# Optimization experiments

Measured on AMD Instinct MI355X. Metric: run time of the kernel, lower is better.

## Reference

```python
import jax, jax.numpy as jnp
import numpy as np

RANGE_MIN = -5.0
RANGE_MAX = 5.0
NBINS = 32
N, D = 1 << 20, 64
MIN_SLOPE = 1e-8


def setup_inputs() -> dict:
    key = jax.random.key(0)
    k1, k2, k3, k4 = jax.random.split(key, 4)
    interval = RANGE_MAX - RANGE_MIN
    min_bin_width = interval / NBINS / 100.0  # __init__ default
    # samples, mostly inside [range_min, range_max]
    x = (jax.random.normal(k1, (N, D), jnp.float32) * 2.0)
    # constrained params, produced exactly as the TransformedVariable bijectors do:
    # bin widths/heights: Shift(min_bin_width) o Scale(interval - mbw*nbins) o SoftmaxCentered
    def softmax_centered(u):
        pad = jnp.zeros(u.shape[:-1] + (1,), u.dtype)
        return jax.nn.softmax(jnp.concatenate([u, pad], axis=-1), axis=-1)
    scale = interval - min_bin_width * NBINS
    uw = 0.1 * jax.random.normal(k2, (D, NBINS - 1))
    uh = 0.1 * jax.random.normal(k3, (D, NBINS - 1))
    us = 0.01 * jax.random.normal(k4, (D, NBINS - 1))
    bin_widths = (min_bin_width + scale * softmax_centered(uw)).astype(jnp.float32)   # [D, nbins]
    bin_heights = (min_bin_width + scale * softmax_centered(uh)).astype(jnp.float32)  # [D, nbins]
    knot_slopes = (MIN_SLOPE + jax.nn.softplus(us)).astype(jnp.float32)               # [D, nbins-1]
    return {"x": x, "bin_widths": bin_widths, "bin_heights": bin_heights,
            "knot_slopes": knot_slopes}


def _spline_1d(x, kx, ky, kd):
    """Rational-quadratic spline forward for one dimension.
    x: [N]; kx, ky: [nbins+1] knot positions; kd: [nbins+1] knot slopes."""
    nbins = kx.shape[0] - 1
    # bin index k s.t. kx[k] <= x < kx[k+1]
    idx = jnp.clip(jnp.searchsorted(kx, x, side='right') - 1, 0, nbins - 1)
    xk, xk1 = kx[idx], kx[idx + 1]
    yk, yk1 = ky[idx], ky[idx + 1]
    dk, dk1 = kd[idx], kd[idx + 1]
    w = xk1 - xk
    h = yk1 - yk
    s = h / w                      # bin mean slope
    t = (x - xk) / w               # relative position in bin
    tt = t * (1.0 - t)
    num = h * (s * t * t + dk * tt)
    den = s + (dk1 + dk - 2.0 * s) * tt
    y = yk + num / den
    # TFP: identity outside [range_min, range_max]
    inside = (x >= kx[0]) & (x <= kx[-1])
    return jnp.where(inside, y, x)


def reference(x, bin_widths, bin_heights, knot_slopes):
    d = x.shape[-1]
    zeros = jnp.zeros((d, 1), x.dtype)
    ones = jnp.ones((d, 1), x.dtype)
    kx = RANGE_MIN + jnp.concatenate([zeros, jnp.cumsum(bin_widths, axis=-1)], axis=-1)   # [D, nbins+1]
    ky = RANGE_MIN + jnp.concatenate([zeros, jnp.cumsum(bin_heights, axis=-1)], axis=-1)  # [D, nbins+1]
    kd = jnp.concatenate([ones, knot_slopes, ones], axis=-1)  # boundary slopes fixed to 1
    return jax.vmap(_spline_1d, in_axes=(1, 0, 0, 0), out_axes=1)(x, kx, ky, kd)
```

## Files before the change

### kernel.cpp

```cpp
#include <hip/hip_runtime.h>

#define NBINS 32
#define DIM 64
#define RANGE_MIN_F (-5.0f)
#define RANGE_MAX_F (5.0f)
#define NCELL 64
#define LUT_STRIDE 68
#define BLOCK 512
#define GRID 768
#define INV_CW 6.4f
#define GBIAS 32.0f

typedef float f32x4 __attribute__((ext_vector_type(4)));


__global__ __launch_bounds__(BLOCK, 6) void rqs_fused(
        const float* __restrict__ x,
        const float* __restrict__ bw,
        const float* __restrict__ bh,
        const float* __restrict__ ks,
        float* __restrict__ out,
        int total) {
    __shared__ float4 s_recA[DIM * NBINS];
    __shared__ float2 s_kd2[DIM * NBINS];
    __shared__ unsigned char s_lut[DIM * LUT_STRIDE];

    const int t = threadIdx.x;

    if (t < DIM) {
        const int d = t;
        const int sw = d >> 2;
        float accw = 0.0f, acch = 0.0f;
        #pragma unroll
        for (int k = 0; k < NBINS; ++k) {
            float w = bw[d * NBINS + k];
            float h = bh[d * NBINS + k];
            s_recA[d * NBINS + ((k + sw) & (NBINS - 1))] =
                make_float4(RANGE_MIN_F + accw, __builtin_amdgcn_rcpf(w),
                            RANGE_MIN_F + acch, h);
            accw += w; acch += h;
        }
    } else if (t < 2 * DIM) {
        const int d = t - DIM;
        const int sw = d >> 2;
        float prev = 1.0f;
        #pragma unroll
        for (int k = 0; k < NBINS; ++k) {
            float nxt = (k < NBINS - 1) ? ks[d * (NBINS - 1) + k] : 1.0f;
            s_kd2[d * NBINS + ((k + sw) & (NBINS - 1))] = make_float2(prev, nxt);
            prev = nxt;
        }
    }
    __syncthreads();

    const float cellw = (RANGE_MAX_F - RANGE_MIN_F) / (float)NCELL;
    #pragma unroll
    for (int e = 0; e < (DIM * NCELL + BLOCK - 1) / BLOCK; ++e) {
        int j = t + e * BLOCK;
        if (j < DIM * NCELL) {
            int d = j >> 6, g = j & (NCELL - 1);
            int sw = d >> 2;
            float cl = RANGE_MIN_F + (float)g * cellw;
            int p = 0;
            #pragma unroll
            for (int s = 16; s >= 1; s >>= 1) {
                float kxs = s_recA[d * NBINS + ((p + s + sw) & (NBINS - 1))].x;
                p += (kxs <= cl) ? s : 0;
            }
            s_lut[d * LUT_STRIDE + g] = (unsigned char)p;
        }
    }
    __syncthreads();

    auto eval1 = [&](float xv, int d) -> float {
        const int sw = d >> 2;
        float gf = fmaf(xv, INV_CW, GBIAS);
        gf = fminf(fmaxf(gf, 0.0f), (float)(NCELL - 1));
        int g = (int)gf;
        int p = (int)s_lut[d * LUT_STRIDE + g];
        int ix1 = d * NBINS + ((p + sw) & (NBINS - 1));
        int ix2 = d * NBINS + ((p + 1 + sw) & (NBINS - 1));
        float4 a1 = s_recA[ix1];
        float4 a2 = s_recA[ix2];
        float2 b1 = s_kd2[ix1];
        float2 b2 = s_kd2[ix2];
        float t1 = (xv - a1.x) * a1.y;
        float t2 = (xv - a2.x) * a2.y;
        bool adv = (t1 >= 1.0f) && (p < NBINS - 1);
        float tt0 = adv ? t2 : t1;
        float yk  = adv ? a2.z : a1.z;
        float h   = adv ? a2.w : a1.w;
        float iw  = adv ? a2.y : a1.y;
        float dk  = adv ? b2.x : b1.x;
        float dk1 = adv ? b2.y : b1.y;
        int pp = p + (adv ? 1 : 0);
        while (__builtin_expect((tt0 >= 1.0f) && (pp < NBINS - 1), 0)) {
            ++pp;
            int ixf = d * NBINS + ((pp + sw) & (NBINS - 1));
            float4 aa = s_recA[ixf];
            float2 bb = s_kd2[ixf];
            tt0 = (xv - aa.x) * aa.y;
            yk = aa.z; h = aa.w; iw = aa.y; dk = bb.x; dk1 = bb.y;
        }
        float sm  = h * iw;
        float tt  = tt0 * (1.0f - tt0);
        float num = h * fmaf(dk, tt, sm * tt0 * tt0);
        float den = fmaf(fmaf(-2.0f, sm, dk + dk1), tt, sm);
        float y   = fmaf(num, __builtin_amdgcn_rcpf(den), yk);
        bool inside = (xv >= RANGE_MIN_F) && (tt0 <= 1.0f);
        return inside ? y : xv;
    };

    auto eval4 = [&](f32x4 c, int d0) -> f32x4 {
        f32x4 r;
        r[0] = eval1(c[0], d0 + 0);
        r[1] = eval1(c[1], d0 + 1);
        r[2] = eval1(c[2], d0 + 2);
        r[3] = eval1(c[3], d0 + 3);
        return r;
    };

    const int tid  = blockIdx.x * BLOCK + t;
    const int TOTV = GRID * BLOCK;
    const int d0   = (4 * tid) & (DIM - 1);
    const int nvec = total >> 2;
    const f32x4* X4 = (const f32x4*)x;
    f32x4* O4 = (f32x4*)out;

    int v = tid;
    if (v < nvec) {
        f32x4 c0 = __builtin_nontemporal_load(&X4[v]);
        bool has1 = (v + TOTV < nvec);
        f32x4 c1 = c0;
        if (has1) c1 = __builtin_nontemporal_load(&X4[v + TOTV]);
        while (true) {
            int v2 = v + 2 * TOTV;
            bool m0 = (v2 < nvec);
            bool m1 = (v2 + TOTV < nvec);
            f32x4 p0 = c0, p1 = c1;
            if (m0) p0 = __builtin_nontemporal_load(&X4[v2]);
            if (m1) p1 = __builtin_nontemporal_load(&X4[v2 + TOTV]);
            f32x4 r0 = eval4(c0, d0);
            __builtin_nontemporal_store(r0, &O4[v]);
            if (has1) {
                f32x4 r1 = eval4(c1, d0);
                __builtin_nontemporal_store(r1, &O4[v + TOTV]);
            }
            if (!m0) break;
            c0 = p0; c1 = p1; has1 = m1; v = v2;
        }
    }
    int rem = total & 3;
    if (rem && tid < rem) {
        int i = (total & ~3) + tid;
        out[i] = eval1(x[i], i & (DIM - 1));
    }
}

extern "C" void kernel_launch(void* const* d_in, const int* in_sizes, int n_in,
                              void* d_out, int out_size, void* d_ws, size_t ws_size,
                              hipStream_t stream) {
    const float* x  = (const float*)d_in[0];
    const float* bw = (const float*)d_in[1];
    const float* bh = (const float*)d_in[2];
    const float* ks = (const float*)d_in[3];
    float* out = (float*)d_out;

    rqs_fused<<<GRID, BLOCK, 0, stream>>>(x, bw, bh, ks, out, out_size);
}
```

Before: 439.3 us.

## Repack spline knot tables into float2 bounds and float4 record with fp16 slopes

Splits the per-bin shared memory tables into a float2 of knot x bounds and a float4 holding inverse width, y knot, height and the two slopes packed as half2. Bin selection uses the float2 bounds, then a single float4 record is fetched for the chosen bin. This replaces four LDS reads per element with two, lowering LDS bandwidth pressure. The second read now depends on the first, and storing slopes in fp16 reduces their precision.

```diff
diff --git a/kernel.cpp b/kernel.cpp
--- a/kernel.cpp
+++ b/kernel.cpp
@@ -1,4 +1,5 @@
 #include <hip/hip_runtime.h>
+#include <hip/hip_fp16.h>
 
 #define NBINS 32
 #define DIM 64
@@ -21,34 +22,36 @@
         const float* __restrict__ ks,
         float* __restrict__ out,
         int total) {
-    __shared__ float4 s_recA[DIM * NBINS];
-    __shared__ float2 s_kd2[DIM * NBINS];
+    __shared__ float2 s_ap[DIM * NBINS];
+    __shared__ float4 s_b [DIM * NBINS];
     __shared__ unsigned char s_lut[DIM * LUT_STRIDE];
 
     const int t = threadIdx.x;
 
     if (t < DIM) {
-        const int d = t;
-        const int sw = d >> 2;
-        float accw = 0.0f, acch = 0.0f;
+        const int d = t, sw = d >> 2;
+        float acc = 0.0f;
         #pragma unroll
         for (int k = 0; k < NBINS; ++k) {
             float w = bw[d * NBINS + k];
-            float h = bh[d * NBINS + k];
-            s_recA[d * NBINS + ((k + sw) & (NBINS - 1))] =
-                make_float4(RANGE_MIN_F + accw, __builtin_amdgcn_rcpf(w),
-                            RANGE_MIN_F + acch, h);
-            accw += w; acch += h;
+            int s = d * NBINS + ((k + sw) & (NBINS - 1));
+            s_ap[s] = make_float2(RANGE_MIN_F + acc, RANGE_MIN_F + acc + w);
+            s_b[s].x = __builtin_amdgcn_rcpf(w);
+            acc += w;
         }
     } else if (t < 2 * DIM) {
-        const int d = t - DIM;
-        const int sw = d >> 2;
-        float prev = 1.0f;
+        const int d = t - DIM, sw = d >> 2;
+        float acc = 0.0f, prev = 1.0f;
         #pragma unroll
         for (int k = 0; k < NBINS; ++k) {
+            float h = bh[d * NBINS + k];
             float nxt = (k < NBINS - 1) ? ks[d * (NBINS - 1) + k] : 1.0f;
-            s_kd2[d * NBINS + ((k + sw) & (NBINS - 1))] = make_float2(prev, nxt);
-            prev = nxt;
+            int s = d * NBINS + ((k + sw) & (NBINS - 1));
+            s_b[s].y = RANGE_MIN_F + acc;
+            s_b[s].z = h;
+            __half2 hp = __floats2half2_rn(prev, nxt);
+            s_b[s].w = __builtin_bit_cast(float, hp);
+            acc += h; prev = nxt;
         }
     }
     __syncthreads();
@@ -64,7 +67,7 @@
             int p = 0;
             #pragma unroll
             for (int s = 16; s >= 1; s >>= 1) {
-                float kxs = s_recA[d * NBINS + ((p + s + sw) & (NBINS - 1))].x;
+                float kxs = s_ap[d * NBINS + ((p + s + sw) & (NBINS - 1))].x;
                 p += (kxs <= cl) ? s : 0;
             }
             s_lut[d * LUT_STRIDE + g] = (unsigned char)p;
@@ -78,30 +81,23 @@
         gf = fminf(fmaxf(gf, 0.0f), (float)(NCELL - 1));
         int g = (int)gf;
         int p = (int)s_lut[d * LUT_STRIDE + g];
-        int ix1 = d * NBINS + ((p + sw) & (NBINS - 1));
-        int ix2 = d * NBINS + ((p + 1 + sw) & (NBINS - 1));
-        float4 a1 = s_recA[ix1];
-        float4 a2 = s_recA[ix2];
-        float2 b1 = s_kd2[ix1];
-        float2 b2 = s_kd2[ix2];
-        float t1 = (xv - a1.x) * a1.y;
-        float t2 = (xv - a2.x) * a2.y;
-        bool adv = (t1 >= 1.0f) && (p < NBINS - 1);
-        float tt0 = adv ? t2 : t1;
-        float yk  = adv ? a2.z : a1.z;
-        float h   = adv ? a2.w : a1.w;
-        float iw  = adv ? a2.y : a1.y;
-        float dk  = adv ? b2.x : b1.x;
-        float dk1 = adv ? b2.y : b1.y;
-        int pp = p + (adv ? 1 : 0);
-        while (__builtin_expect((tt0 >= 1.0f) && (pp < NBINS - 1), 0)) {
-            ++pp;
-            int ixf = d * NBINS + ((pp + sw) & (NBINS - 1));
-            float4 aa = s_recA[ixf];
-            float2 bb = s_kd2[ixf];
-            tt0 = (xv - aa.x) * aa.y;
-            yk = aa.z; h = aa.w; iw = aa.y; dk = bb.x; dk1 = bb.y;
+        float2 ap = s_ap[d * NBINS + ((p + sw) & (NBINS - 1))];
+        bool adv = (xv >= ap.y) && (p < NBINS - 1);
+        int sel = p + (adv ? 1 : 0);
+        float xks = adv ? ap.y : ap.x;
+        float4 b = s_b[d * NBINS + ((sel + sw) & (NBINS - 1))];
+        float tt0 = (xv - xks) * b.x;
+        while (__builtin_expect((tt0 >= 1.0f) && (sel < NBINS - 1), 0)) {
+            ++sel;
+            int ix = d * NBINS + ((sel + sw) & (NBINS - 1));
+            xks = s_ap[ix].x;
+            b = s_b[ix];
+            tt0 = (xv - xks) * b.x;
         }
+        __half2 hp = __builtin_bit_cast(__half2, b.w);
+        float dk  = __low2float(hp);
+        float dk1 = __high2float(hp);
+        float iw = b.x, yk = b.y, h = b.z;
         float sm  = h * iw;
         float tt  = tt0 * (1.0f - tt0);
         float num = h * fmaf(dk, tt, sm * tt0 * tt0);
```

Measured after the change: 466.4 us. 6.2% more time.
